# Kernel tuning notes

Hardware: AMD Instinct MI355X
Metric: run time of the kernel (lower is better)

The kernel has to match this reference:

```python
import jax, jax.numpy as jnp
import numpy as np

ALPHA = 32.0
EPS = 1e-8
NEG_SLOPE = 0.01  # torch F.leaky_relu default


def setup_inputs() -> dict:
    key = jax.random.key(0)
    k_x, k_h, k_a, k_b, k_c, k_d = jax.random.split(key, 6)
    B, S, D_IN, D_OUT, R = 4, 4096, 4096, 4096, 16
    std = 1.0 / np.sqrt(R)
    return {
        "x": jax.random.normal(k_x, (B, S, D_IN), dtype=jnp.float32),
        "h_t": jax.random.uniform(k_h, (B, S, R), dtype=jnp.float32),
        "W_a": jax.random.normal(k_a, (D_IN, R), dtype=jnp.float32) * std,
        "W_b": jax.random.normal(k_b, (R, D_OUT), dtype=jnp.float32) * std,
        "W_c": jax.random.normal(k_c, (R, R), dtype=jnp.float32) * std,
        "W_d": jax.random.normal(k_d, (R, R), dtype=jnp.float32) * std,
    }


def reference(x, h_t, W_a, W_b, W_c, W_d):
    # x: [B,S,in_dim]; h_t: [B,S,rank] (recurrent state already shape-matched)
    new_x = jnp.einsum("bsd,dr->bsr", x, W_a)            # [B,S,R]
    h_t1 = h_t @ W_c + new_x @ W_d + h_t                  # [B,S,R]
    # min-max normalization over the rank axis (dim=2)
    min_val = jnp.min(h_t1, axis=2, keepdims=True)
    max_val = jnp.max(h_t1, axis=2, keepdims=True)
    h_norm = (h_t1 - min_val) / (max_val - min_val + EPS)
    # dropout in eval mode (identity); leaky_relu with torch default slope
    act = jnp.where(h_norm >= 0, h_norm, NEG_SLOPE * h_norm)
    y = ALPHA * jnp.einsum("bsr,ro->bso", new_x + act, W_b)  # [B,S,out_dim]
    return y
```

## Files before the change

kernel.cpp:

```cpp
#include <hip/hip_runtime.h>

#define ALPHA_F 32.0f
#define EPS_F 1e-8f
#define NEG_SLOPE_F 0.01f

#define D_IN 4096
#define D_OUT 4096
#define RNK 16
#define N_ROWS 16384
#define ROWS_PER_BLOCK 16
#define THREADS 256

__global__ __launch_bounds__(THREADS) void ssm_lora_fused(
    const float* __restrict__ x,
    const float* __restrict__ h_t,
    const float* __restrict__ Wa,
    const float* __restrict__ Wb,
    const float* __restrict__ Wc,
    const float* __restrict__ Wd,
    float* __restrict__ y)
{
    __shared__ float red[4][16][68];
    __shared__ float lds_nx[16][16];
    __shared__ float lds_u[16][16];

    const int tid  = threadIdx.x;
    const int lane = tid & 63;
    const int w    = tid >> 6;
    const long row0 = (long)blockIdx.x * ROWS_PER_BLOCK;
    const int wr0  = w * 4;

    float acc[4][16];
    #pragma unroll
    for (int rr = 0; rr < 4; ++rr)
        #pragma unroll
        for (int r = 0; r < 16; ++r) acc[rr][r] = 0.0f;

    const float4* x4 = (const float4*)x;
    const long xbase = (row0 + wr0) * (D_IN / 4);

    for (int k = 0; k < 16; ++k) {
        const int p = lane + (k << 6);
        float4 xv[4];
        #pragma unroll
        for (int rr = 0; rr < 4; ++rr)
            xv[rr] = x4[xbase + (long)rr * (D_IN / 4) + p];

        #pragma unroll
        for (int dd = 0; dd < 4; ++dd) {
            const float4* war = (const float4*)(Wa + ((size_t)(4 * p + dd) << 4));
            const float4 w0 = war[0], w1 = war[1], w2 = war[2], w3 = war[3];
            #pragma unroll
            for (int rr = 0; rr < 4; ++rr) {
                const float xs = ((const float*)&xv[rr])[dd];
                acc[rr][0]  += xs * w0.x;  acc[rr][1]  += xs * w0.y;
                acc[rr][2]  += xs * w0.z;  acc[rr][3]  += xs * w0.w;
                acc[rr][4]  += xs * w1.x;  acc[rr][5]  += xs * w1.y;
                acc[rr][6]  += xs * w1.z;  acc[rr][7]  += xs * w1.w;
                acc[rr][8]  += xs * w2.x;  acc[rr][9]  += xs * w2.y;
                acc[rr][10] += xs * w2.z;  acc[rr][11] += xs * w2.w;
                acc[rr][12] += xs * w3.x;  acc[rr][13] += xs * w3.y;
                acc[rr][14] += xs * w3.z;  acc[rr][15] += xs * w3.w;
            }
        }
    }

    #pragma unroll
    for (int rr = 0; rr < 4; ++rr)
        #pragma unroll
        for (int r = 0; r < 16; ++r) {
            float v = acc[rr][r];
            v += __shfl_xor(v, 1, 64);
            v += __shfl_xor(v, 2, 64);
            acc[rr][r] = v;
        }
    if ((lane & 3) == 0) {
        const int li = lane >> 2;
        #pragma unroll
        for (int rr = 0; rr < 4; ++rr)
            #pragma unroll
            for (int r = 0; r < 16; ++r)
                red[w][li][rr * 16 + r] = acc[rr][r];
    }
    __syncthreads();

    {
        const int row  = tid >> 4;
        const int r    = tid & 15;
        const int w2   = tid >> 6;
        const int slot = tid & 63;
        float s = 0.0f;
        #pragma unroll
        for (int i = 0; i < 16; ++i) s += red[w2][i][slot];
        lds_nx[row][r] = s;
        __syncthreads();

        const float* hrow = h_t + (row0 + row) * RNK;
        float h1 = hrow[r];
        #pragma unroll
        for (int j = 0; j < 16; ++j)
            h1 += hrow[j] * Wc[j * 16 + r] + lds_nx[row][j] * Wd[j * 16 + r];

        float mn = h1, mx = h1;
        #pragma unroll
        for (int m = 1; m <= 8; m <<= 1) {
            mn = fminf(mn, __shfl_xor(mn, m, 64));
            mx = fmaxf(mx, __shfl_xor(mx, m, 64));
        }
        const float hn = (h1 - mn) / (mx - mn + EPS_F);
        const float a  = (hn >= 0.0f) ? hn : NEG_SLOPE_F * hn;
        lds_u[row][r] = ALPHA_F * (s + a);
    }
    __syncthreads();

    float4 uu[4][4];
    #pragma unroll
    for (int rr = 0; rr < 4; ++rr)
        #pragma unroll
        for (int j = 0; j < 4; ++j)
            uu[rr][j] = ((const float4*)lds_u[wr0 + rr])[j];

    const float4* Wb4 = (const float4*)Wb;
    float4* y4 = (float4*)y;
    const long ybase = (row0 + wr0) * (D_OUT / 4);

    for (int k = 0; k < 16; ++k) {
        const int p = lane + (k << 6);
        float4 wb[16];
        #pragma unroll
        for (int r2 = 0; r2 < 16; ++r2) wb[r2] = Wb4[(size_t)r2 * 1024 + p];
        #pragma unroll
        for (int rr = 0; rr < 4; ++rr) {
            float4 o; o.x = 0.0f; o.y = 0.0f; o.z = 0.0f; o.w = 0.0f;
            #pragma unroll
            for (int r2 = 0; r2 < 16; ++r2) {
                const float us = ((const float*)&uu[rr][0])[r2];
                o.x += us * wb[r2].x;
                o.y += us * wb[r2].y;
                o.z += us * wb[r2].z;
                o.w += us * wb[r2].w;
            }
            y4[ybase + (long)rr * (D_OUT / 4) + p] = o;
        }
    }
}

extern "C" void kernel_launch(void* const* d_in, const int* in_sizes, int n_in,
                              void* d_out, int out_size, void* d_ws, size_t ws_size,
                              hipStream_t stream) {
    const float* x   = (const float*)d_in[0];
    const float* h_t = (const float*)d_in[1];
    const float* Wa  = (const float*)d_in[2];
    const float* Wb  = (const float*)d_in[3];
    const float* Wc  = (const float*)d_in[4];
    const float* Wd  = (const float*)d_in[5];
    float* y = (float*)d_out;

    dim3 grid(N_ROWS / ROWS_PER_BLOCK);
    dim3 block(THREADS);
    ssm_lora_fused<<<grid, block, 0, stream>>>(x, h_t, Wa, Wb, Wc, Wd, y);
}
```

Measured before the change: 654.8 us.

## Split fused LoRA kernel into transpose, down-projection and up-projection stages

Splits the single fused kernel into three launches. The first transposes W_a into workspace. The second computes the rank-16 projection plus the recurrent, normalisation and activation step per row, using a lower-register layout (each 16-lane group owns one row and reduces with a butterfly shuffle), and writes u to workspace. The third streams W_b to produce y. The goal is to raise occupancy and drop the large LDS reduction in the x-read phase; the cost is two extra launches and a small round trip of u through memory. The fused kernel stays as a fallback when workspace is missing.

Result: slower. 741.2 us (+13.2%).

```diff
diff --git a/kernel.cpp b/kernel.cpp
--- a/kernel.cpp
+++ b/kernel.cpp
@@ -8,10 +8,128 @@
 #define D_OUT 4096
 #define RNK 16
 #define N_ROWS 16384
-#define ROWS_PER_BLOCK 16
-#define THREADS 256
-
-__global__ __launch_bounds__(THREADS) void ssm_lora_fused(
+
+__global__ __launch_bounds__(256) void wa_transpose(
+    const float* __restrict__ Wa, float* __restrict__ WaT)
+{
+    const int idx = blockIdx.x * 256 + threadIdx.x;
+    const int d = idx & (D_IN - 1);
+    const int r = idx >> 12;
+    WaT[idx] = Wa[d * RNK + r];
+}
+
+__global__ __launch_bounds__(256, 4) void ssm_stage1(
+    const float* __restrict__ x,
+    const float* __restrict__ h_t,
+    const float* __restrict__ WaT,
+    const float* __restrict__ Wc,
+    const float* __restrict__ Wd,
+    float* __restrict__ u)
+{
+    const int tid  = threadIdx.x;
+    const int lane = tid & 63;
+    const int w    = tid >> 6;
+    const int g    = lane >> 4;
+    const int q    = lane & 15;
+    const long row = (long)blockIdx.x * 16 + w * 4 + g;
+
+    const float4* x4  = (const float4*)x + row * (D_IN / 4);
+    const float4* wt4 = (const float4*)WaT;
+
+    float acc[RNK];
+    #pragma unroll
+    for (int r = 0; r < RNK; ++r) acc[r] = 0.0f;
+
+    #pragma unroll 2
+    for (int k = 0; k < 64; ++k) {
+        const int p = q + (k << 4);
+        const float4 xv = x4[p];
+        #pragma unroll
+        for (int r = 0; r < RNK; ++r) {
+            const float4 wv = wt4[r * (D_IN / 4) + p];
+            acc[r] += xv.x * wv.x + xv.y * wv.y + xv.z * wv.z + xv.w * wv.w;
+        }
+    }
+
+    #pragma unroll
+    for (int s = 0; s < 4; ++s) {
+        const int m = 1 << s;
+        const bool up = (lane & m) != 0;
+        #pragma unroll
+        for (int i = 0; i < (8 >> s); ++i) {
+            const float a0 = acc[2 * i], a1 = acc[2 * i + 1];
+            const float mine = up ? a1 : a0;
+            const float send = up ? a0 : a1;
+            acc[i] = mine + __shfl_xor(send, m, 64);
+        }
+    }
+    const float nx = acc[0];
+
+    const float h_own = h_t[row * RNK + q];
+    float h1 = 0.0f;
+    #pragma unroll
+    for (int j = 0; j < RNK; ++j) {
+        const float hj  = __shfl(h_own, j, 16);
+        const float nxj = __shfl(nx, j, 16);
+        const float wc  = Wc[j * RNK + q] + ((j == q) ? 1.0f : 0.0f);
+        h1 += hj * wc + nxj * Wd[j * RNK + q];
+    }
+
+    float mn = h1, mx = h1;
+    #pragma unroll
+    for (int m = 1; m <= 8; m <<= 1) {
+        mn = fminf(mn, __shfl_xor(mn, m, 64));
+        mx = fmaxf(mx, __shfl_xor(mx, m, 64));
+    }
+    const float hn = (h1 - mn) / (mx - mn + EPS_F);
+    const float a  = (hn >= 0.0f) ? hn : NEG_SLOPE_F * hn;
+    u[row * RNK + q] = ALPHA_F * (nx + a);
+}
+
+__global__ __launch_bounds__(256) void ssm_stage2(
+    const float* __restrict__ u,
+    const float* __restrict__ Wb,
+    float* __restrict__ y)
+{
+    const int tid  = threadIdx.x;
+    const int lane = tid & 63;
+    const int w    = tid >> 6;
+    const long row0 = (long)blockIdx.x * 16 + w * 4;
+
+    float4 uu[4][4];
+    #pragma unroll
+    for (int rr = 0; rr < 4; ++rr) {
+        const float4* ur = (const float4*)(u + (row0 + rr) * RNK);
+        #pragma unroll
+        for (int j = 0; j < 4; ++j) uu[rr][j] = ur[j];
+    }
+
+    const float4* Wb4 = (const float4*)Wb;
+    float4* y4 = (float4*)y;
+    const long ybase = row0 * (D_OUT / 4);
+
+    for (int k = 0; k < 16; ++k) {
+        const int p = lane + (k << 6);
+        float4 wb[16];
+        #pragma unroll
+        for (int r2 = 0; r2 < 16; ++r2) wb[r2] = Wb4[(size_t)r2 * 1024 + p];
+        #pragma unroll
+        for (int rr = 0; rr < 4; ++rr) {
+            float4 o; o.x = 0.0f; o.y = 0.0f; o.z = 0.0f; o.w = 0.0f;
+            #pragma unroll
+            for (int r2 = 0; r2 < 16; ++r2) {
+                const float us = ((const float*)&uu[rr][0])[r2];
+                o.x += us * wb[r2].x;
+                o.y += us * wb[r2].y;
+                o.z += us * wb[r2].z;
+                o.w += us * wb[r2].w;
+            }
+            y4[ybase + (long)rr * (D_OUT / 4) + p] = o;
+        }
+    }
+}
+
+__global__ __launch_bounds__(256) void ssm_lora_fused(
     const float* __restrict__ x,
     const float* __restrict__ h_t,
     const float* __restrict__ Wa,
@@ -27,7 +145,7 @@
     const int tid  = threadIdx.x;
     const int lane = tid & 63;
     const int w    = tid >> 6;
-    const long row0 = (long)blockIdx.x * ROWS_PER_BLOCK;
+    const long row0 = (long)blockIdx.x * 16;
     const int wr0  = w * 4;
 
     float acc[4][16];
@@ -156,7 +274,14 @@
     const float* Wd  = (const float*)d_in[5];
     float* y = (float*)d_out;
 
-    dim3 grid(N_ROWS / ROWS_PER_BLOCK);
-    dim3 block(THREADS);
-    ssm_lora_fused<<<grid, block, 0, stream>>>(x, h_t, Wa, Wb, Wc, Wd, y);
-}
+    const size_t need = (size_t)(RNK * D_IN + (size_t)N_ROWS * RNK) * sizeof(float);
+    if (d_ws != nullptr && ws_size >= need) {
+        float* WaT = (float*)d_ws;
+        float* u   = WaT + (size_t)RNK * D_IN;
+        wa_transpose<<<dim3((RNK * D_IN) / 256), dim3(256), 0, stream>>>(Wa, WaT);
+        ssm_stage1<<<dim3(N_ROWS / 16), dim3(256), 0, stream>>>(x, h_t, WaT, Wc, Wd, u);
+        ssm_stage2<<<dim3(N_ROWS / 16), dim3(256), 0, stream>>>(u, Wb, y);
+    } else {
+        ssm_lora_fused<<<dim3(N_ROWS / 16), dim3(256), 0, stream>>>(x, h_t, Wa, Wb, Wc, Wd, y);
+    }
+}
```
